# Kernel tuning notes

Hardware: AMD Instinct MI355X
Metric: run time of the kernel (lower is better)

Reference implementation:

```python
import jax, jax.numpy as jnp
import numpy as np

HEADS = 24
HEAD_DIM = 96
SPARSE_N = 4
ROPE_FREQ = 10000.0


def _rope_axis(x, pos, scale):
    # x: (s, b, h, D) with D even; pos: (s,) integer positions along one axis
    D = x.shape[-1]
    inv_freq = 1.0 / (ROPE_FREQ ** (jnp.arange(0, D, 2, dtype=jnp.float32) / D))
    t = pos.astype(jnp.float32) / scale
    freqs = t[:, None] * inv_freq[None, :]            # (s, D/2)
    emb = jnp.concatenate([freqs, freqs], axis=-1)    # (s, D)
    cos = jnp.cos(emb)[:, None, None, :]              # broadcast over (b, h)
    sin = jnp.sin(emb)[:, None, None, :]
    x1, x2 = jnp.split(x, 2, axis=-1)
    rot = jnp.concatenate([-x2, x1], axis=-1)         # rotate_half
    return x * cos + rot * sin


def _rope3d(x, frame, height, width, scales=(1.0, 1.0, 1.0)):
    # x: (s, b, h, d); head dim is split into 3 equal chunks for t/h/w axes
    s, b, h, d = x.shape
    D = d // 3
    tt, hh, ww = jnp.meshgrid(jnp.arange(frame), jnp.arange(height), jnp.arange(width), indexing='ij')
    pos_t, pos_h, pos_w = tt.reshape(-1), hh.reshape(-1), ww.reshape(-1)
    return jnp.concatenate([
        _rope_axis(x[..., :D], pos_t, scales[0]),
        _rope_axis(x[..., D:2 * D], pos_h, scales[1]),
        _rope_axis(x[..., 2 * D:], pos_w, scales[2]),
    ], axis=-1)


def setup_inputs() -> dict:
    key = jax.random.key(0)
    ks = jax.random.split(key, 9)
    frame, height, width, b = 8, 16, 16, 4
    s = frame * height * width          # 2048
    dim = HEADS * HEAD_DIM              # 2304
    w_scale = 0.02
    return {
        'hidden_states': jax.random.normal(ks[0], (s, b, dim), jnp.float32),
        'wq': jax.random.normal(ks[1], (dim, dim), jnp.float32) * w_scale,
        'bq': jnp.zeros((dim,), jnp.float32),
        'wk': jax.random.normal(ks[2], (dim, dim), jnp.float32) * w_scale,
        'bk': jnp.zeros((dim,), jnp.float32),
        'wv': jax.random.normal(ks[3], (dim, dim), jnp.float32) * w_scale,
        'bv': jnp.zeros((dim,), jnp.float32),
        'wo': jax.random.normal(ks[4], (dim, dim), jnp.float32) * w_scale,
        'bo': jnp.zeros((dim,), jnp.float32),
        'frame': frame,
        'height': height,
        'width': width,
    }


def reference(hidden_states, wq, bq, wk, bk, wv, bv, wo, bo, frame, height, width):
    # hidden_states: (s, b, dim) in SBH layout, self-attention path (no seq-parallel)
    s, b, dim = hidden_states.shape
    n = SPARSE_N

    q = hidden_states @ wq + bq
    k = hidden_states @ wk + bk
    v = hidden_states @ wv + bv

    # 3D RoPE on q/k, per-head
    q = _rope3d(q.reshape(s, b, HEADS, HEAD_DIM), frame, height, width).reshape(s, b, dim)
    k = _rope3d(k.reshape(s, b, HEADS, HEAD_DIM), frame, height, width).reshape(s, b, dim)

    # _sparse_1d (sparse_group=False): pad s to multiple of n*n, then
    # '(g k) b d -> g (k b) d' == contiguous reshape
    pad_len = (-s) % (n * n)
    sp_s = (s + pad_len) // n
    sp_b = n * b

    def sparse(x):
        if pad_len:
            x = jnp.pad(x, ((0, pad_len), (0, 0), (0, 0)))
        return x.reshape(sp_s, sp_b, dim)

    q, k, v = sparse(q), sparse(k), sparse(v)

    # 's b (h d) -> b h s d'
    def to_bhsd(x):
        return x.reshape(sp_s, sp_b, HEADS, HEAD_DIM).transpose(1, 2, 0, 3)

    qh, kh, vh = to_bhsd(q), to_bhsd(k), to_bhsd(v)

    # scaled dot-product attention (no mask, no dropout, non-causal)
    scale = HEAD_DIM ** -0.5
    scores = jnp.einsum('bhqd,bhkd->bhqk', qh, kh) * scale
    attn = jax.nn.softmax(scores, axis=-1)
    out = jnp.einsum('bhqk,bhkd->bhqd', attn, vh)

    # 'b h s d -> s b (h d)', reverse sparse rearrange, drop padding
    out = out.transpose(2, 0, 1, 3).reshape(sp_s, sp_b, dim)
    out = out.reshape(sp_s * n, b, dim)[:s]

    # to_out[0] linear, to_out[1] dropout (identity in eval), rescale_output_factor=1
    return out @ wo + bo
```

## Files before the change

kernel.cpp:

```cpp
#include <hip/hip_runtime.h>
#include <hip/hip_bf16.h>

typedef __attribute__((ext_vector_type(8))) __bf16 bf16x8;
typedef __attribute__((ext_vector_type(4))) __bf16 bf16x4;
typedef __attribute__((ext_vector_type(4))) float  f32x4;

#define DIM   2304
#define NH    24
#define HD    96
#define SPS   512

__device__ __forceinline__ void gload16(const void* gp, void* lp) {
  __builtin_amdgcn_global_load_lds(
      (__attribute__((address_space(1))) void*)(unsigned long long)gp,
      (__attribute__((address_space(3))) void*)lp, 16, 0, 0);
}

__global__ __launch_bounds__(256) void prep_kernel(
    const float* __restrict__ hs,
    const float* __restrict__ wq, const float* __restrict__ wk,
    const float* __restrict__ wv, const float* __restrict__ wo,
    __bf16* __restrict__ hsb, __bf16* __restrict__ wqkvT, __bf16* __restrict__ woT)
{
  __shared__ float t[64][65];
  const int bid = blockIdx.x;
  const int tid = threadIdx.x;
  if (bid < 5184) {
    const int z = bid / 1296;
    const int rest = bid - z * 1296;
    const int n0 = (rest % 36) * 64, k0 = (rest / 36) * 64;
    const float* src = (z == 0) ? wq : (z == 1) ? wk : (z == 2) ? wv : wo;
    __bf16* dst = (z < 3) ? (wqkvT + (size_t)z * DIM * DIM) : woT;
    const int tx = tid & 63, ty = tid >> 6;
#pragma unroll
    for (int j = 0; j < 64; j += 4)
      t[ty + j][tx] = src[(size_t)(k0 + ty + j) * DIM + n0 + tx];
    __syncthreads();
#pragma unroll
    for (int j = 0; j < 64; j += 4)
      dst[(size_t)(n0 + ty + j) * DIM + k0 + tx] = (__bf16)t[tx][ty + j];
  } else {
    const int i = (bid - 5184) * 256 + tid;
    const float4 f = ((const float4*)hs)[i];
    bf16x4 o = { (__bf16)f.x, (__bf16)f.y, (__bf16)f.z, (__bf16)f.w };
    ((bf16x4*)hsb)[i] = o;
  }
}


template<int NJ>
__device__ __forceinline__ void stage_half(
    const __bf16* __restrict__ X, __bf16* lX, int r0, int k0,
    int srow, int schunk, int dslot)
{
#pragma unroll
  for (int j = 0; j < NJ; ++j)
    gload16(X + (size_t)(r0 + j * 64 + srow) * DIM + k0 + schunk,
            lX + (j * 64 + srow) * 64 + dslot);
}

template<int EPI, int MF, int GRID>
__global__ __launch_bounds__(512, 2) void gemm8p_kernel(
    const __bf16* __restrict__ A, const __bf16* __restrict__ B,
    const float* __restrict__ b0, const float* __restrict__ b1, const float* __restrict__ b2,
    __bf16* __restrict__ o0, __bf16* __restrict__ o1, __bf16* __restrict__ o2,
    float* __restrict__ fout)
{
  constexpr int MROWS = MF * 64;
  constexpr int VG = MF + 4;
  __shared__ __align__(16) __bf16 As[2][MROWS * 64];
  __shared__ __align__(16) __bf16 Bs[2][256 * 64];
  __shared__ float tcos[640], tsin[640];
  const int tid = threadIdx.x;
  if (EPI == 0) {
    for (int i = tid; i < 640; i += 512) {
      int pos, jj = i & 15;
      if (i < 128)      pos = i >> 4;
      else if (i < 384) pos = (i - 128) >> 4;
      else              pos = (i - 384) >> 4;
      const float invf = exp2f(-(float)jj * 0.83048202372184059f);
      float s, c;
      sincosf((float)pos * invf, &s, &c);
      tcos[i] = c; tsin[i] = s;
    }
  }
  const int wid = tid >> 6, l = tid & 63;
  const int lq = l & 15, lg = l >> 4;
  const int wm = wid >> 2, wn = wid & 3;
  const int bid = blockIdx.x;
  const int xcd = bid & 7, local = bid >> 3;
  int m0, n0;
  if (GRID == 0) {
    m0 = (xcd * 4 + (local & 3)) * 256;
    n0 = (local >> 2) * 256;
  } else if (GRID == 1) {
    m0 = (xcd * 4 + ((local >> 1) & 3)) * 256 + (local & 1) * 128;
    n0 = (24 + (local >> 3)) * 256;
  } else if (GRID == 2) {
    m0 = (xcd * 8 + (local & 7)) * 128;
    n0 = (local >> 3) * 256;
  } else {
    m0 = (xcd * 8 + (local >> 1)) * 128 + (local & 1) * 64;
    n0 = 2048;
  }
  const int srow = tid >> 3;
  const int schunk = ((tid & 7) ^ (srow & 7)) * 8;
  const int dslot = (tid & 7) * 8;
  const int laneA0 = lq * 128 + ((lg * 16) ^ ((lq & 7) << 4));
  const int laneA1 = lq * 128 + ((64 + lg * 16) ^ ((lq & 7) << 4));

  f32x4 acc[2 * MF][4] = {};
  bf16x8 a[MF][2], b0r[2][2], b1r[2][2];

#define LOAD_A(APx, Hh) do { _Pragma("unroll")                                   \
  for (int fm = 0; fm < MF; ++fm) {                                              \
    a[fm][0] = *(const bf16x8*)((APx) + (wm * (MF * 32) + (Hh) * (MF * 16) + fm * 16) * 128 + laneA0); \
    a[fm][1] = *(const bf16x8*)((APx) + (wm * (MF * 32) + (Hh) * (MF * 16) + fm * 16) * 128 + laneA1); } } while (0)

#define LOAD_B(dst, BPx, Qq) do { _Pragma("unroll")                              \
  for (int fn = 0; fn < 2; ++fn) {                                               \
    dst[fn][0] = *(const bf16x8*)((BPx) + (wn * 64 + (Qq) * 32 + fn * 16) * 128 + laneA0); \
    dst[fn][1] = *(const bf16x8*)((BPx) + (wn * 64 + (Qq) * 32 + fn * 16) * 128 + laneA1); } } while (0)

#define MFMA_C(bset, Hh, Qq) do { __builtin_amdgcn_s_setprio(1); _Pragma("unroll") \
  for (int fm = 0; fm < MF; ++fm) _Pragma("unroll")                              \
    for (int fn = 0; fn < 2; ++fn) _Pragma("unroll")                             \
      for (int kk = 0; kk < 2; ++kk)                                             \
        acc[(Hh) * MF + fm][(Qq) * 2 + fn] = __builtin_amdgcn_mfma_f32_16x16x32_bf16( \
            a[fm][kk], bset[fn][kk], acc[(Hh) * MF + fm][(Qq) * 2 + fn], 0, 0, 0); \
  __builtin_amdgcn_s_setprio(0); } while (0)

  stage_half<MF>(A, As[0], m0, 0, srow, schunk, dslot);
  stage_half<4>(B, Bs[0], n0, 0, srow, schunk, dslot);
  stage_half<MF>(A, As[1], m0, 64, srow, schunk, dslot);
  stage_half<4>(B, Bs[1], n0, 64, srow, schunk, dslot);
  asm volatile("s_waitcnt vmcnt(%0)" :: "n"(VG) : "memory");
  __builtin_amdgcn_s_barrier();

  const char* a0p = (const char*)&As[0][0];
  const char* b0p = (const char*)&Bs[0][0];
  const char* a1p = (const char*)&As[1][0];
  const char* b1p = (const char*)&Bs[1][0];

#define TILE_STAGED(AP, BP, SA, SB, KN)                                          \
  LOAD_A(AP, 0); LOAD_B(b0r, BP, 0); LOAD_B(b1r, BP, 1);                         \
  __builtin_amdgcn_s_barrier();                                                  \
  MFMA_C(b0r, 0, 0);                                                             \
  __builtin_amdgcn_s_barrier();                                                  \
  MFMA_C(b1r, 0, 1);                                                             \
  LOAD_A(AP, 1);                                                                 \
  __builtin_amdgcn_s_barrier();                                                  \
  stage_half<4>(B, SB, n0, KN, srow, schunk, dslot);                             \
  MFMA_C(b1r, 1, 1);                                                             \
  __builtin_amdgcn_s_barrier();                                                  \
  stage_half<MF>(A, SA, m0, KN, srow, schunk, dslot);                            \
  MFMA_C(b0r, 1, 0);                                                             \
  asm volatile("s_waitcnt vmcnt(%0)" :: "n"(VG) : "memory");                     \
  __builtin_amdgcn_s_barrier();

#define TILE_PLAIN(AP, BP)                                                       \
  LOAD_A(AP, 0); LOAD_B(b0r, BP, 0); LOAD_B(b1r, BP, 1);                         \
  __builtin_amdgcn_s_barrier();                                                  \
  MFMA_C(b0r, 0, 0);                                                             \
  __builtin_amdgcn_s_barrier();                                                  \
  MFMA_C(b1r, 0, 1);                                                             \
  LOAD_A(AP, 1);                                                                 \
  __builtin_amdgcn_s_barrier();                                                  \
  MFMA_C(b1r, 1, 1);                                                             \
  __builtin_amdgcn_s_barrier();                                                  \
  MFMA_C(b0r, 1, 0);

  for (int tt = 0; tt < 34; tt += 2) {
    TILE_STAGED(a0p, b0p, As[0], Bs[0], (tt + 2) * 64)
    TILE_STAGED(a1p, b1p, As[1], Bs[1], (tt + 3) * 64)
  }
  TILE_PLAIN(a0p, b0p)
  asm volatile("s_waitcnt vmcnt(0)" ::: "memory");
  __builtin_amdgcn_s_barrier();
  TILE_PLAIN(a1p, b1p)
#undef TILE_STAGED
#undef TILE_PLAIN
#undef LOAD_A
#undef LOAD_B
#undef MFMA_C

  if (EPI == 0) {
    const int mat = n0 / DIM;
    const int nb = n0 - mat * DIM;
    const float* bias = (mat == 0) ? b0 : (mat == 1) ? b1 : b2;
    __bf16* outp = (mat == 0) ? o0 : (mat == 1) ? o1 : o2;
#pragma unroll
    for (int mr = 0; mr < 2 * MF; ++mr) {
      const int gq = (m0 + wm * (MF * 32) + mr * 16) >> 4;
      const int si = gq * 4 + lg;
      const int pos3[3] = { si >> 8, (si >> 4) & 15, si & 15 };
#pragma unroll
      for (int p = 0; p < 2; ++p) {
        const int nlo = nb + wn * 64 + (2 * p) * 16 + lq;
        const int nhi = nlo + 16;
        const int hlo = nlo / HD, dlo = nlo - hlo * HD;
        const int hhi = nhi / HD, dhi = nhi - hhi * HD;
        const float blo = bias[nlo], bhi = bias[nhi];
        float c = 1.f, s = 0.f;
        if (mat < 2) {
          const int cix = dlo >> 5;
          const int toff = ((cix == 0) ? 0 : (cix == 1) ? 128 : 384) + pos3[cix] * 16 + lq;
          c = tcos[toff]; s = tsin[toff];
        }
#pragma unroll
        for (int r = 0; r < 4; ++r) {
          const int bp = lg * 4 + r;
          const float x1 = acc[mr][2 * p][r] + blo;
          const float x2 = acc[mr][2 * p + 1][r] + bhi;
          float y1 = x1, y2 = x2;
          if (mat < 2) { y1 = x1 * c - x2 * s; y2 = x2 * c + x1 * s; }
          outp[((size_t)(bp * NH + hlo) * SPS + gq) * HD + dlo] = (__bf16)y1;
          outp[((size_t)(bp * NH + hhi) * SPS + gq) * HD + dhi] = (__bf16)y2;
        }
      }
    }
  } else {
#pragma unroll
    for (int mr = 0; mr < 2 * MF; ++mr) {
      const int rbase = m0 + wm * (MF * 32) + mr * 16;
#pragma unroll
      for (int nr = 0; nr < 4; ++nr) {
        const int n = n0 + wn * 64 + nr * 16 + lq;
        const float bia = b0[n];
#pragma unroll
        for (int r = 0; r < 4; ++r)
          fout[(size_t)(rbase + lg * 4 + r) * DIM + n] = acc[mr][nr][r] + bia;
      }
    }
  }
}

__global__ __launch_bounds__(256) void transpose_v_kernel(
    const __bf16* __restrict__ v, __bf16* __restrict__ vT)
{
  __shared__ __bf16 t[96][72];
  const int tid = threadIdx.x, bid = blockIdx.x;
  const int bh = bid >> 3, g0 = (bid & 7) * 64;
  const __bf16* src = v + ((size_t)bh * SPS + g0) * HD;
#pragma unroll
  for (int it = 0; it < 3; ++it) {
    const int lin = it * 256 + tid;
    const int row = lin / 12, c8 = (lin % 12) * 8;
    bf16x8 x = *(const bf16x8*)(src + row * HD + c8);
#pragma unroll
    for (int j = 0; j < 8; ++j) {
      const int d = c8 + j;
      t[d][row ^ ((d & 7) << 3)] = x[j];
    }
  }
  __syncthreads();
  __bf16* dst = vT + (size_t)bh * HD * SPS + g0;
#pragma unroll
  for (int it = 0; it < 3; ++it) {
    const int lin = it * 256 + tid;
    const int d = lin / 8, gc = (lin % 8) * 8;
    bf16x8 o = *(const bf16x8*)&t[d][gc ^ ((d & 7) << 3)];
    *(bf16x8*)(dst + (size_t)d * SPS + (gc ^ ((d & 7) << 3))) = o;
  }
}

__global__ __launch_bounds__(256) void attn_kernel(
    const __bf16* __restrict__ q, const __bf16* __restrict__ k,
    const __bf16* __restrict__ vTs, __bf16* __restrict__ ao)
{
  __shared__ __align__(16) __bf16 Kt[2][64 * 96];
  __shared__ __align__(16) __bf16 Vt[2][96 * 64];
  __shared__ __bf16 Pl[4][16 * 72];
  const int tid = threadIdx.x;
  const int w = tid >> 6, l = tid & 63;
  const int lq = l & 15, lg = l >> 4;
  const int bid = blockIdx.x;
  const int swz = (bid & 7) * 384 + (bid >> 3);
  const int qt = swz & 7;
  const int h  = (swz >> 3) % NH;
  const int bp = swz / (NH * 8);
  const size_t bh = (size_t)bp * NH + h;
  const __bf16* qb = q + bh * SPS * HD;
  const char* kbytes = (const char*)(k + bh * SPS * HD);
  const __bf16* vb = vTs + bh * HD * SPS;
  const int vrow = w * 24 + (l >> 3);
  const int vcol = (l & 7) * 8;
  bf16x8 qf[3];
  {
    const __bf16* qr = qb + (size_t)(qt * 64 + w * 16 + lq) * HD + lg * 8;
    qf[0] = *(const bf16x8*)(qr);
    qf[1] = *(const bf16x8*)(qr + 32);
    qf[2] = *(const bf16x8*)(qr + 64);
  }
  const float sc = 0.10206207261596575f * 1.4426950408889634f;
  float m_run = -1e30f, l_run = 0.f;
  f32x4 o[6] = {};
#pragma unroll
  for (int j = 0; j < 3; ++j)
    gload16(kbytes + j * 4096 + tid * 16, (char*)&Kt[0][0] + j * 4096 + tid * 16);
#pragma unroll
  for (int j = 0; j < 3; ++j)
    gload16(vb + (size_t)(vrow + j * 8) * SPS + vcol,
            &Vt[0][(vrow + j * 8) * 64 + vcol]);

  for (int t = 0; t < 8; ++t) {
    const int cur = t & 1;
    const int kb0 = t * 64;
    __builtin_amdgcn_s_barrier();
    if (t < 7) {
#pragma unroll
      for (int j = 0; j < 3; ++j)
        gload16(kbytes + (size_t)(kb0 + 64) * 192 + j * 4096 + tid * 16,
                (char*)&Kt[1 - cur][0] + j * 4096 + tid * 16);
#pragma unroll
      for (int j = 0; j < 3; ++j)
        gload16(vb + (size_t)(vrow + j * 8) * SPS + (kb0 + 64) + vcol,
                &Vt[1 - cur][(vrow + j * 8) * 64 + vcol]);
      asm volatile("s_waitcnt vmcnt(6)" ::: "memory");
    } else {
      asm volatile("s_waitcnt vmcnt(0)" ::: "memory");
    }
    __builtin_amdgcn_s_barrier();
    f32x4 st[4];
    __builtin_amdgcn_s_setprio(1);
#pragma unroll
    for (int t2 = 0; t2 < 4; ++t2) {
      const __bf16* kr = &Kt[cur][(t2 * 16 + lq) * 96 + lg * 8];
      bf16x8 k0f = *(const bf16x8*)(kr);
      bf16x8 k1f = *(const bf16x8*)(kr + 32);
      bf16x8 k2f = *(const bf16x8*)(kr + 64);
      f32x4 s = {};
      s = __builtin_amdgcn_mfma_f32_16x16x32_bf16(k0f, qf[0], s, 0, 0, 0);
      s = __builtin_amdgcn_mfma_f32_16x16x32_bf16(k1f, qf[1], s, 0, 0, 0);
      s = __builtin_amdgcn_mfma_f32_16x16x32_bf16(k2f, qf[2], s, 0, 0, 0);
      st[t2] = s;
    }
    __builtin_amdgcn_s_setprio(0);
    float pmax = -1e30f;
#pragma unroll
    for (int t2 = 0; t2 < 4; ++t2)
#pragma unroll
      for (int r = 0; r < 4; ++r) pmax = fmaxf(pmax, st[t2][r]);
    pmax *= sc;
    if (__any(pmax > m_run + 8.f)) {
      float mn = fmaxf(m_run, pmax);
      mn = fmaxf(mn, __shfl_xor(mn, 16));
      mn = fmaxf(mn, __shfl_xor(mn, 32));
      const float alpha = exp2f(m_run - mn);
      l_run *= alpha;
      float al[4];
#pragma unroll
      for (int r = 0; r < 4; ++r) al[r] = __shfl(alpha, lg * 4 + r);
#pragma unroll
      for (int ni = 0; ni < 6; ++ni)
#pragma unroll
        for (int r = 0; r < 4; ++r) o[ni][r] *= al[r];
      m_run = mn;
    }
#pragma unroll
    for (int t2 = 0; t2 < 4; ++t2) {
      bf16x4 pb;
#pragma unroll
      for (int r = 0; r < 4; ++r) {
        const float p = exp2f(st[t2][r] * sc - m_run);
        l_run += p;
        pb[r] = (__bf16)p;
      }
      *(bf16x4*)&Pl[w][lq * 72 + t2 * 16 + lg * 4] = pb;
    }
#pragma unroll
    for (int ks = 0; ks < 2; ++ks) {
      bf16x8 pa = *(const bf16x8*)&Pl[w][lq * 72 + ks * 32 + lg * 8];
      __builtin_amdgcn_s_setprio(1);
#pragma unroll
      for (int ni = 0; ni < 6; ++ni) {
        const int col = (ks * 32 + lg * 8) ^ ((lq & 7) << 3);
        bf16x8 vf = *(const bf16x8*)&Vt[cur][(ni * 16 + lq) * 64 + col];
        o[ni] = __builtin_amdgcn_mfma_f32_16x16x32_bf16(pa, vf, o[ni], 0, 0, 0);
      }
      __builtin_amdgcn_s_setprio(0);
    }
  }
  l_run += __shfl_xor(l_run, 16);
  l_run += __shfl_xor(l_run, 32);
  float linv[4];
#pragma unroll
  for (int r = 0; r < 4; ++r) linv[r] = 1.f / __shfl(l_run, lg * 4 + r);
#pragma unroll
  for (int ni = 0; ni < 6; ++ni)
#pragma unroll
    for (int r = 0; r < 4; ++r) {
      const int gq = qt * 64 + w * 16 + lg * 4 + r;
      const int d = ni * 16 + lq;
      ao[(size_t)(gq * 16 + bp) * DIM + h * HD + d] = (__bf16)(o[ni][r] * linv[r]);
    }
}

extern "C" void kernel_launch(void* const* d_in, const int* in_sizes, int n_in,
                              void* d_out, int out_size, void* d_ws, size_t ws_size,
                              hipStream_t stream) {
  const float* hs = (const float*)d_in[0];
  const float* wq = (const float*)d_in[1];
  const float* bq = (const float*)d_in[2];
  const float* wk = (const float*)d_in[3];
  const float* bk = (const float*)d_in[4];
  const float* wv = (const float*)d_in[5];
  const float* bv = (const float*)d_in[6];
  const float* wo = (const float*)d_in[7];
  const float* bo = (const float*)d_in[8];
  float* out = (float*)d_out;

  char* ws = (char*)d_ws;
  __bf16* wqkvT = (__bf16*)(ws);
  __bf16* hsb   = (__bf16*)(ws + 31850496);
  __bf16* qb    = (__bf16*)(ws + 69599232);
  __bf16* kbuf  = (__bf16*)(ws + 107347968);
  __bf16* vbuf  = (__bf16*)(ws + 145096704);
  __bf16* woT   = (__bf16*)(ws + 182845440);
  __bf16* vbufT = (__bf16*)(ws);
  __bf16* ao    = vbuf;

  prep_kernel<<<23616, 256, 0, stream>>>(hs, wq, wk, wv, wo, hsb, wqkvT, woT);
  gemm8p_kernel<0, 4, 0><<<768, 512, 0, stream>>>(hsb, wqkvT, bq, bk, bv, qb, kbuf, vbuf, nullptr);
  gemm8p_kernel<0, 2, 1><<<192, 512, 0, stream>>>(hsb, wqkvT, bq, bk, bv, qb, kbuf, vbuf, nullptr);
  transpose_v_kernel<<<3072, 256, 0, stream>>>(vbuf, vbufT);
  attn_kernel<<<3072, 256, 0, stream>>>(qb, kbuf, vbufT, ao);
  gemm8p_kernel<1, 2, 2><<<512, 512, 0, stream>>>(ao, woT, bo, nullptr, nullptr, nullptr, nullptr, nullptr, out);
  gemm8p_kernel<1, 1, 3><<<128, 512, 0, stream>>>(ao, woT, bo, nullptr, nullptr, nullptr, nullptr, nullptr, out);
}
```

Measured before the change: 492.1 us.

## Use 128-query attention blocks of 8 waves sharing K/V tiles

Doubles the attention block from 4 to 8 waves, so each block covers 128 queries and each staged K/V tile in LDS is reused by twice as many waves. The grid is halved and the block-index swizzle recomputed to match. The prefetch schedule is also restructured: the next tile is issued at the start of each iteration and a full vmcnt(0) wait plus barrier sits at the end, replacing the partial-wait double barrier. This reduces global K/V traffic per query but gives up partial-wait overlap and halves the number of blocks available to fill the GPU.

```diff
diff --git a/kernel.cpp b/kernel.cpp
--- a/kernel.cpp
+++ b/kernel.cpp
@@ -264,30 +264,28 @@
   }
 }
 
-__global__ __launch_bounds__(256) void attn_kernel(
+__global__ __launch_bounds__(512, 2) void attn_kernel(
     const __bf16* __restrict__ q, const __bf16* __restrict__ k,
     const __bf16* __restrict__ vTs, __bf16* __restrict__ ao)
 {
   __shared__ __align__(16) __bf16 Kt[2][64 * 96];
   __shared__ __align__(16) __bf16 Vt[2][96 * 64];
-  __shared__ __bf16 Pl[4][16 * 72];
+  __shared__ __bf16 Pl[8][16 * 72];
   const int tid = threadIdx.x;
   const int w = tid >> 6, l = tid & 63;
   const int lq = l & 15, lg = l >> 4;
   const int bid = blockIdx.x;
-  const int swz = (bid & 7) * 384 + (bid >> 3);
-  const int qt = swz & 7;
-  const int h  = (swz >> 3) % NH;
-  const int bp = swz / (NH * 8);
+  const int swz = (bid & 7) * 192 + (bid >> 3);
+  const int qt = swz & 3;
+  const int h  = (swz >> 2) % NH;
+  const int bp = swz / (NH * 4);
   const size_t bh = (size_t)bp * NH + h;
   const __bf16* qb = q + bh * SPS * HD;
   const char* kbytes = (const char*)(k + bh * SPS * HD);
-  const __bf16* vb = vTs + bh * HD * SPS;
-  const int vrow = w * 24 + (l >> 3);
-  const int vcol = (l & 7) * 8;
+  const char* vbytes = (const char*)(vTs + bh * HD * SPS);
   bf16x8 qf[3];
   {
-    const __bf16* qr = qb + (size_t)(qt * 64 + w * 16 + lq) * HD + lg * 8;
+    const __bf16* qr = qb + (size_t)(qt * 128 + w * 16 + lq) * HD + lg * 8;
     qf[0] = *(const bf16x8*)(qr);
     qf[1] = *(const bf16x8*)(qr + 32);
     qf[2] = *(const bf16x8*)(qr + 64);
@@ -295,32 +293,26 @@
   const float sc = 0.10206207261596575f * 1.4426950408889634f;
   float m_run = -1e30f, l_run = 0.f;
   f32x4 o[6] = {};
-#pragma unroll
-  for (int j = 0; j < 3; ++j)
-    gload16(kbytes + j * 4096 + tid * 16, (char*)&Kt[0][0] + j * 4096 + tid * 16);
-#pragma unroll
-  for (int j = 0; j < 3; ++j)
-    gload16(vb + (size_t)(vrow + j * 8) * SPS + vcol,
-            &Vt[0][(vrow + j * 8) * 64 + vcol]);
+
+#define STAGE_TILE(tt, buf) do {                                                  \
+    const int s0 = tid;                                                           \
+    gload16(kbytes + (size_t)(tt) * 12288 + s0 * 16, (char*)&Kt[buf][0] + s0 * 16); \
+    gload16(vbytes + (size_t)(s0 >> 3) * 1024 + (tt) * 128 + (s0 & 7) * 16,       \
+            (char*)&Vt[buf][0] + s0 * 16);                                        \
+    if (w < 4) {                                                                  \
+      const int s1 = 512 + tid;                                                   \
+      gload16(kbytes + (size_t)(tt) * 12288 + s1 * 16, (char*)&Kt[buf][0] + s1 * 16); \
+      gload16(vbytes + (size_t)(s1 >> 3) * 1024 + (tt) * 128 + (s1 & 7) * 16,     \
+              (char*)&Vt[buf][0] + s1 * 16);                                      \
+    } } while (0)
+
+  STAGE_TILE(0, 0);
+  asm volatile("s_waitcnt vmcnt(0)" ::: "memory");
+  __builtin_amdgcn_s_barrier();
 
   for (int t = 0; t < 8; ++t) {
     const int cur = t & 1;
-    const int kb0 = t * 64;
-    __builtin_amdgcn_s_barrier();
-    if (t < 7) {
-#pragma unroll
-      for (int j = 0; j < 3; ++j)
-        gload16(kbytes + (size_t)(kb0 + 64) * 192 + j * 4096 + tid * 16,
-                (char*)&Kt[1 - cur][0] + j * 4096 + tid * 16);
-#pragma unroll
-      for (int j = 0; j < 3; ++j)
-        gload16(vb + (size_t)(vrow + j * 8) * SPS + (kb0 + 64) + vcol,
-                &Vt[1 - cur][(vrow + j * 8) * 64 + vcol]);
-      asm volatile("s_waitcnt vmcnt(6)" ::: "memory");
-    } else {
-      asm volatile("s_waitcnt vmcnt(0)" ::: "memory");
-    }
-    __builtin_amdgcn_s_barrier();
+    if (t < 7) STAGE_TILE(t + 1, 1 - cur);
     f32x4 st[4];
     __builtin_amdgcn_s_setprio(1);
 #pragma unroll
@@ -380,7 +372,10 @@
       }
       __builtin_amdgcn_s_setprio(0);
     }
-  }
+    asm volatile("s_waitcnt vmcnt(0)" ::: "memory");
+    __builtin_amdgcn_s_barrier();
+  }
+#undef STAGE_TILE
   l_run += __shfl_xor(l_run, 16);
   l_run += __shfl_xor(l_run, 32);
   float linv[4];
@@ -390,7 +385,7 @@
   for (int ni = 0; ni < 6; ++ni)
 #pragma unroll
     for (int r = 0; r < 4; ++r) {
-      const int gq = qt * 64 + w * 16 + lg * 4 + r;
+      const int gq = qt * 128 + w * 16 + lg * 4 + r;
       const int d = ni * 16 + lq;
       ao[(size_t)(gq * 16 + bp) * DIM + h * HD + d] = (__bf16)(o[ni][r] * linv[r]);
     }
@@ -424,7 +419,7 @@
   gemm8p_kernel<0, 4, 0><<<768, 512, 0, stream>>>(hsb, wqkvT, bq, bk, bv, qb, kbuf, vbuf, nullptr);
   gemm8p_kernel<0, 2, 1><<<192, 512, 0, stream>>>(hsb, wqkvT, bq, bk, bv, qb, kbuf, vbuf, nullptr);
   transpose_v_kernel<<<3072, 256, 0, stream>>>(vbuf, vbufT);
-  attn_kernel<<<3072, 256, 0, stream>>>(qb, kbuf, vbufT, ao);
+  attn_kernel<<<1536, 512, 0, stream>>>(qb, kbuf, vbufT, ao);
   gemm8p_kernel<1, 2, 2><<<512, 512, 0, stream>>>(ao, woT, bo, nullptr, nullptr, nullptr, nullptr, nullptr, out);
   gemm8p_kernel<1, 1, 3><<<128, 512, 0, stream>>>(ao, woT, bo, nullptr, nullptr, nullptr, nullptr, nullptr, out);
 }
```

After: 474.1 us. -3.7%, faster.
